# Optimization experiments

Measured on AMD Instinct MI355X. Metric: run time of the kernel, lower is better.

The kernel has to match this reference:

```python
import jax, jax.numpy as jnp
import numpy as np
import math

B, C, H, W = 8, 64, 256, 256
E, NH = 256, 8
HD = E // NH  # 32


def get_coords(h, w):
    xx, yy = jnp.meshgrid(jnp.arange(h, dtype=jnp.float32), jnp.arange(w, dtype=jnp.float32), indexing='ij')
    return jnp.stack((xx.reshape(-1), yy.reshape(-1)), axis=-1)  # [N, 2]


def setup_inputs() -> dict:
    key = jax.random.key(0)
    ks = jax.random.split(key, 12)
    def xavier(k, shape):
        fan_out, fan_in = shape
        a = math.sqrt(6.0 / (fan_in + fan_out))
        return jax.random.uniform(k, shape, jnp.float32, -a, a)
    x = jax.random.normal(ks[0], (B, C, H, W), jnp.float32)
    z = jax.random.normal(ks[1], (B, C), jnp.float32)
    pos = jax.random.uniform(ks[2], (B, NH, 2), jnp.float32) * (H - 1)
    Wq = xavier(ks[3], (E, C)); bq = jnp.zeros((E,), jnp.float32)
    Wk = xavier(ks[4], (E, C)); bk = jnp.zeros((E,), jnp.float32)
    Wv = xavier(ks[5], (E, C)); bv = jnp.zeros((E,), jnp.float32)
    Wp = xavier(ks[6], (HD, 2)); bp = jax.random.uniform(ks[7], (HD,), jnp.float32, -1.0, 1.0) / math.sqrt(2.0)
    return {"x": x, "z": z, "pos": pos, "Wq": Wq, "bq": bq, "Wk": Wk, "bk": bk,
            "Wv": Wv, "bv": bv, "Wp": Wp, "bp": bp}


def reference(x, z, pos, Wq, bq, Wk, bk, Wv, bv, Wp, bp):
    b, c, h, w = x.shape
    n = h * w
    x_flat = x.reshape(b, c, n).transpose(0, 2, 1)          # [B, N, C]
    pos_grid = get_coords(h, w)                              # [N, 2]
    q = (z @ Wq.T + bq).reshape(b, NH, HD)                   # [B, H, hd]
    k = (x_flat @ Wk.T + bk).reshape(b, n, NH, HD)           # [B, N, H, hd]
    # relative-position modulation of keys
    rel = pos_grid[None, :, None, :] - pos[:, None, :, :]    # [B, N, H, 2]
    qxk = rel @ Wp.T + bp                                    # [B, N, H, hd]
    k = k * qxk
    v = x_flat @ Wv.T + bv                                   # [B, N, E]
    attn_logits = jnp.einsum('bhc,bnhc->bnh', q, k) / math.sqrt(HD)
    attention = jax.nn.softmax(attn_logits, axis=1)          # softmax over N
    pos_out = jnp.einsum('bnh,nx->bhx', attention, pos_grid) # [B, H, 2]
    values = jnp.einsum('bnh,bnc->bhc', attention, v)        # [B, H, E]
    return (values, pos_out)
```

## Files before the change

### kernel.cpp

```cpp
#include <hip/hip_runtime.h>

#define NN    65536
#define NSUB  128
#define NBLK  (NN/NSUB)

typedef short bf16x8 __attribute__((ext_vector_type(8)));
typedef float f32x4v __attribute__((ext_vector_type(4)));
typedef unsigned short ushort_t;
typedef unsigned int uint_t;

#define XHI_B  0
#define XLO_B  18432
#define SLICE  4608
#define LGSTR  28
#define PSTR   40
#define PST_OFF 1536
#define RED_B  36864
#define SMEM_BYTES 37248

#define WTHI_B  0
#define WTLO_B  32768
#define CJ_B    65536
#define PM_B    66304
#define PL_B    197376
#define PSP_B   328448
#define PSX_B   590592
#define Q_B     8979200
#define QSTR    68

__device__ __forceinline__ uint_t bf16_rne_bits(float f) {
  uint_t u = __float_as_uint(f);
  return (u + 0x7FFFu + ((u >> 16) & 1u)) >> 16;
}
__device__ __forceinline__ uint_t cvt_pk_bf16(float a, float b) {
  uint_t r;
  asm("v_cvt_pk_bf16_f32 %0, %1, %2" : "=v"(r) : "v"(a), "v"(b));
  return r;
}
template <int CTRL, int RMASK = 0xf>
__device__ __forceinline__ float dpp_add(float x) {
  int t = __builtin_amdgcn_update_dpp(0, __float_as_int(x), CTRL, RMASK, 0xf, false);
  return x + __int_as_float(t);
}
template <int CTRL, int RMASK = 0xf>
__device__ __forceinline__ float dpp_maxs(float x) {
  int t = __builtin_amdgcn_update_dpp((int)0xFF800000u, __float_as_int(x), CTRL, RMASK, 0xf, false);
  return fmaxf(x, __int_as_float(t));
}
__device__ __forceinline__ float half_sum(float x) {
  x = dpp_add<0x111>(x); x = dpp_add<0x112>(x); x = dpp_add<0x114>(x);
  x = dpp_add<0x118>(x); x = dpp_add<0x142, 0xA>(x);
  return x;
}
__device__ __forceinline__ float half_max(float x) {
  x = dpp_maxs<0x111>(x); x = dpp_maxs<0x112>(x); x = dpp_maxs<0x114>(x);
  x = dpp_maxs<0x118>(x); x = dpp_maxs<0x142, 0xA>(x);
  return x;
}

__global__ __launch_bounds__(64) void prep_kernel(
    const float* __restrict__ z,  const float* __restrict__ Wq, const float* __restrict__ bq,
    const float* __restrict__ Wk, const float* __restrict__ bk,
    const float* __restrict__ Wp, const float* __restrict__ bp,
    ushort_t* __restrict__ WThi, ushort_t* __restrict__ WTlo, float* __restrict__ Cj)
{
  const int h = blockIdx.x, b = blockIdx.y, t = threadIdx.x;
  __shared__ float q[32];
  if (t < 32) {
    const int e = h*32 + t;
    float a = bq[e];
    const float* zr = z + b*64;
    const float* wr = Wq + e*64;
    #pragma unroll 8
    for (int c = 0; c < 64; ++c) a += zr[c]*wr[c];
    q[t] = a;
  }
  __syncthreads();
  const int c = t;
  float w[3] = {0.f, 0.f, 0.f};
  #pragma unroll 4
  for (int hd = 0; hd < 32; ++hd) {
    const float qk = q[hd] * Wk[(h*32+hd)*64 + c];
    w[0] += qk * bp[hd];
    w[1] += qk * Wp[hd*2+0];
    w[2] += qk * Wp[hd*2+1];
  }
  #pragma unroll
  for (int j = 0; j < 3; ++j) {
    const int coeff = h*3 + j;
    const uint_t hb = bf16_rne_bits(w[j]);
    const float  fh = __uint_as_float(hb << 16);
    const uint_t lb = bf16_rne_bits(w[j] - fh);
    WThi[(b*32 + coeff)*64 + c] = (ushort_t)hb;
    WTlo[(b*32 + coeff)*64 + c] = (ushort_t)lb;
  }
  if (h == 0) {
    #pragma unroll
    for (int r = 0; r < 8; ++r) {
      WThi[(b*32 + 24 + r)*64 + c] = 0;
      WTlo[(b*32 + 24 + r)*64 + c] = 0;
    }
  }
  if (t < 3) {
    float s = 0.f;
    for (int hd = 0; hd < 32; ++hd) {
      const float m = (t == 0) ? bp[hd] : Wp[hd*2 + (t-1)];
      s += q[hd] * m * bk[h*32+hd];
    }
    Cj[b*24 + h*3 + t] = s;
  }
}

__global__ __launch_bounds__(256, 4) void main_kernel(
    const float* __restrict__ x, const float* __restrict__ pos,
    const ushort_t* __restrict__ WThi, const ushort_t* __restrict__ WTlo,
    const float* __restrict__ Cj,
    float* __restrict__ Pm, float* __restrict__ Pl,
    float* __restrict__ Psp, float* __restrict__ Psx)
{
  extern __shared__ char smc[];
  float* red = (float*)(smc + RED_B);
  const int t   = threadIdx.x;
  const int blk = blockIdx.x;
  const int b   = blockIdx.y;
  const int n0  = blk * NSUB;
  const int w   = t >> 6, lid = t & 63;
  const int c0  = lid & 15, q4 = lid >> 4;
  char* slice = smc + XLO_B + w*SLICE;

  bf16x8 bh[2][2], bl[2][2];
  {
    const ushort_t* wtb_h = WThi + b*2048;
    const ushort_t* wtb_l = WTlo + b*2048;
    #pragma unroll
    for (int nt = 0; nt < 2; ++nt)
      #pragma unroll
      for (int ks = 0; ks < 2; ++ks) {
        const int off = (nt*16 + c0)*64 + ks*32 + q4*8;
        bh[nt][ks] = *(const bf16x8*)(wtb_h + off);
        bl[nt][ks] = *(const bf16x8*)(wtb_l + off);
      }
  }

  {
    const int qd  = lid & 7;
    const int g   = lid >> 3;
    const int swz = (4*w + (qd >> 1)) & 7;
    const int chnk = (g ^ swz) * 16;
    const float* xg = x + (size_t)b*64*NN + (size_t)g*8*NN + n0 + w*32 + 4*qd;
    f32x4v v[8];
    #pragma unroll
    for (int j = 0; j < 8; ++j) v[j] = *(const f32x4v*)(xg + (size_t)j*NN);
    #pragma unroll
    for (int i = 0; i < 4; ++i) {
      uint_t H[4], L[4];
      #pragma unroll
      for (int jp = 0; jp < 4; ++jp) {
        const float f0 = v[2*jp][i], f1 = v[2*jp+1][i];
        const uint_t hpk = cvt_pk_bf16(f0, f1);
        const float h0 = __uint_as_float(hpk << 16);
        const float h1 = __uint_as_float(hpk & 0xFFFF0000u);
        const uint_t l0 = __float_as_uint(f0 - h0);
        const uint_t l1 = __float_as_uint(f1 - h1);
        H[jp] = hpk;
        L[jp] = __builtin_amdgcn_perm(l1, l0, 0x07060302u);
      }
      const int row = w*32 + 4*qd + i;
      char* dh = smc + XHI_B + row*144 + chnk;
      char* dl = smc + XLO_B + row*144 + chnk;
      *(uint4*)dh = make_uint4(H[0], H[1], H[2], H[3]);
      *(uint4*)dl = make_uint4(L[0], L[1], L[2], L[3]);
    }
  }

  const int hg  = lid >> 5;
  const int pxl = lid & 31;
  float cj[12];
  {
    const float* cjp = Cj + b*24 + hg*12;
    #pragma unroll
    for (int k = 0; k < 12; ++k) cj[k] = cjp[k];
  }
  const int gx = blk >> 1;
  float rxh[4], py[4];
  #pragma unroll
  for (int hl = 0; hl < 4; ++hl) {
    const int h = hg*4 + hl;
    rxh[hl] = (float)gx - pos[(b*8+h)*2 + 0];
    py[hl]  = pos[(b*8+h)*2 + 1];
  }

  f32x4v acc[2][2];
  #pragma unroll
  for (int mt = 0; mt < 2; ++mt) { acc[mt][0] = (f32x4v)0.f; acc[mt][1] = (f32x4v)0.f; }
  {
    #pragma unroll
    for (int mt = 0; mt < 2; ++mt) {
      const int row  = w*32 + mt*16 + c0;
      const int srow = (4*w + 2*mt + (c0 >> 3)) & 7;
      const int ch0  = (q4 ^ srow) * 16;
      const char* rh = smc + XHI_B + row*144;
      const char* rl = smc + XLO_B + row*144;
      bf16x8 ah0 = *(const bf16x8*)(rh + ch0);
      bf16x8 ah1 = *(const bf16x8*)(rh + (ch0 ^ 64));
      bf16x8 al0 = *(const bf16x8*)(rl + ch0);
      bf16x8 al1 = *(const bf16x8*)(rl + (ch0 ^ 64));
      #pragma unroll
      for (int nt = 0; nt < 2; ++nt) {
        f32x4v a = acc[mt][nt];
        a = __builtin_amdgcn_mfma_f32_16x16x32_bf16(ah0, bh[nt][0], a, 0, 0, 0);
        a = __builtin_amdgcn_mfma_f32_16x16x32_bf16(ah1, bh[nt][1], a, 0, 0, 0);
        a = __builtin_amdgcn_mfma_f32_16x16x32_bf16(ah0, bl[nt][0], a, 0, 0, 0);
        a = __builtin_amdgcn_mfma_f32_16x16x32_bf16(ah1, bl[nt][1], a, 0, 0, 0);
        a = __builtin_amdgcn_mfma_f32_16x16x32_bf16(al0, bh[nt][0], a, 0, 0, 0);
        a = __builtin_amdgcn_mfma_f32_16x16x32_bf16(al1, bh[nt][1], a, 0, 0, 0);
        acc[mt][nt] = a;
      }
    }
  }

  {
    float* lga_w = (float*)slice;
    #pragma unroll
    for (int mt = 0; mt < 2; ++mt)
      #pragma unroll
      for (int r = 0; r < 4; ++r) {
        const int prow = mt*16 + q4*4 + r;
        lga_w[prow*LGSTR + c0] = acc[mt][0][r];
        if (c0 < 8) lga_w[prow*LGSTR + 16 + c0] = acc[mt][1][r];
      }
  }

  float a12[12];
  {
    const float4* ap = (const float4*)((float*)slice + pxl*LGSTR + hg*12);
    #pragma unroll
    for (int r = 0; r < 3; ++r) *(float4*)(a12 + 4*r) = ap[r];
  }
  const float tf = (float)(((blk & 1) << 7) + w*32 + pxl);
  float lg[4];
  #pragma unroll
  for (int hl = 0; hl < 4; ++hl) {
    const float a0 = a12[hl*3+0] + cj[hl*3+0];
    const float a1 = a12[hl*3+1] + cj[hl*3+1];
    const float a2 = a12[hl*3+2] + cj[hl*3+2];
    lg[hl] = (a0 + rxh[hl]*a1 + (tf - py[hl])*a2) * 0.17677669529663687f;
  }

  #pragma unroll
  for (int hl = 0; hl < 4; ++hl) {
    const float m = half_max(lg[hl]);
    if ((lid & 31) == 31) red[w*8 + hg*4 + hl] = m;
  }
  __syncthreads();

  float p[4];
  #pragma unroll
  for (int hl = 0; hl < 4; ++hl) {
    const int h = hg*4 + hl;
    const float M = fmaxf(fmaxf(red[0*8+h], red[1*8+h]), fmaxf(red[2*8+h], red[3*8+h]));
    p[hl] = __expf(lg[hl] - M);
  }

  #pragma unroll
  for (int hl = 0; hl < 4; ++hl) {
    const float sp  = half_sum(p[hl]);
    const float spj = half_sum(p[hl] * tf);
    if ((lid & 31) == 31) {
      red[32 + w*8 + hg*4 + hl] = sp;
      red[64 + w*8 + hg*4 + hl] = spj;
    }
  }
  {
    ushort_t* pls = (ushort_t*)slice;
    #pragma unroll
    for (int hl = 0; hl < 4; ++hl) {
      const int h = hg*4 + hl;
      const uint_t hb = bf16_rne_bits(p[hl]);
      const float  hf = __uint_as_float(hb << 16);
      const uint_t lb = __float_as_uint(p[hl] - hf) >> 16;
      pls[h*PSTR + pxl]     = (ushort_t)hb;
      pls[(h+8)*PSTR + pxl] = (ushort_t)lb;
    }
  }

  {
    const ushort_t* pls = (const ushort_t*)slice;
    const bf16x8 afr = *(const bf16x8*)(pls + c0*PSTR + q4*8);
    const int srow_b = (4*w + q4) & 7;
    float* pst = (float*)(slice + PST_OFF);
    #pragma unroll
    for (int nt = 0; nt < 4; ++nt) {
      const int gch  = nt*2 + (c0 >> 3);
      const char* base = smc + XHI_B + (w*32 + q4*8)*144 + ((gch ^ srow_b)*16) + (c0 & 7)*2;
      bf16x8 bfr;
      #pragma unroll
      for (int j = 0; j < 8; ++j) bfr[j] = *(const short*)(base + j*144);
      f32x4v accB = __builtin_amdgcn_mfma_f32_16x16x32_bf16(afr, bfr, (f32x4v)0.f, 0, 0, 0);
      #pragma unroll
      for (int r = 0; r < 4; ++r) {
        const float o = __shfl_xor(accB[r], 32, 64);
        if (q4 < 2) pst[(q4*4 + r)*64 + nt*16 + c0] = accB[r] + o;
      }
    }
  }
  __syncthreads();

  if (t < 8) {
    const int base = (b*NBLK + blk)*8 + t;
    const float M  = fmaxf(fmaxf(red[0*8+t], red[8+t]), fmaxf(red[16+t], red[24+t]));
    const float L  = red[32+t] + red[40+t] + red[48+t] + red[56+t];
    const float SJ = red[64+t] + red[72+t] + red[80+t] + red[88+t];
    Pm[base] = M;
    Pl[base] = L;
    Psp[base*2+0] = (float)gx * L;
    Psp[base*2+1] = SJ;
  }
  {
    const size_t pb64 = ((size_t)(b*NBLK + blk))*8*64;
    #pragma unroll
    for (int r = 0; r < 2; ++r) {
      const int idx = t + 256*r;
      float s = 0.f;
      #pragma unroll
      for (int w2 = 0; w2 < 4; ++w2)
        s += *(const float*)(smc + XLO_B + w2*SLICE + PST_OFF + idx*4);
      Psx[pb64 + idx] = s;
    }
  }
}

__global__ __launch_bounds__(256) void reduce1_kernel(
    const float* __restrict__ Pm, const float* __restrict__ Pl,
    const float* __restrict__ Psp, const float* __restrict__ Psx,
    float* __restrict__ Q)
{
  const int g = blockIdx.x, h = blockIdx.y, b = blockIdx.z, t = threadIdx.x;
  __shared__ float al[64];
  __shared__ float mgs;
  __shared__ float sums[3];
  __shared__ float sxl[256];
  const int base = (b*NBLK + g*64)*8 + h;

  float m_t = -1e30f;
  if (t < 64) {
    m_t = Pm[base + t*8];
    float mm = m_t;
    #pragma unroll
    for (int off = 32; off >= 1; off >>= 1) mm = fmaxf(mm, __shfl_xor(mm, off, 64));
    if (t == 0) mgs = mm;
  }
  __syncthreads();
  const float Mg = mgs;
  if (t < 64) {
    const float a = __expf(m_t - Mg);
    al[t] = a;
    float lt = Pl[base + t*8] * a;
    float sx = Psp[(base + t*8)*2 + 0] * a;
    float sy = Psp[(base + t*8)*2 + 1] * a;
    #pragma unroll
    for (int off = 32; off >= 1; off >>= 1) {
      lt += __shfl_xor(lt, off, 64);
      sx += __shfl_xor(sx, off, 64);
      sy += __shfl_xor(sy, off, 64);
    }
    if (t == 0) { sums[0] = lt; sums[1] = sx; sums[2] = sy; }
  }
  __syncthreads();
  {
    const int c = t & 63, g2 = t >> 6;
    float acc = 0.f;
    #pragma unroll
    for (int i = 0; i < 16; ++i) {
      const int k = g2*16 + i;
      acc += al[k] * Psx[(size_t)(base + k*8)*64 + c];
    }
    sxl[g2*64 + c] = acc;
  }
  __syncthreads();
  float* q = Q + ((b*8 + h)*8 + g)*QSTR;
  if (t < 64) q[4+t] = sxl[t] + sxl[64+t] + sxl[128+t] + sxl[192+t];
  if (t == 0) { q[0] = Mg; q[1] = sums[0]; q[2] = sums[1]; q[3] = sums[2]; }
}

__global__ __launch_bounds__(64) void reduce2_kernel(
    const float* __restrict__ Q, const float* __restrict__ Wv, const float* __restrict__ bv,
    float* __restrict__ out)
{
  const int h = blockIdx.x, b = blockIdx.y, t = threadIdx.x;
  __shared__ float qm[8], bl[8], l8[8], sx8[8], sy8[8];
  __shared__ float SXs[64];
  const float* qb = Q + ((b*8 + h)*8)*QSTR;

  if (t < 8) qm[t] = qb[t*QSTR + 0];
  __syncthreads();
  float M = qm[0];
  #pragma unroll
  for (int g = 1; g < 8; ++g) M = fmaxf(M, qm[g]);
  if (t < 8) {
    const float be = __expf(qm[t] - M);
    bl[t]  = be;
    l8[t]  = be * qb[t*QSTR + 1];
    sx8[t] = be * qb[t*QSTR + 2];
    sy8[t] = be * qb[t*QSTR + 3];
  }
  __syncthreads();
  float L = 0.f;
  #pragma unroll
  for (int g = 0; g < 8; ++g) L += l8[g];
  const float invL = 1.0f / L;
  {
    float s = 0.f;
    #pragma unroll
    for (int g = 0; g < 8; ++g) s += bl[g] * qb[g*QSTR + 4 + t];
    SXs[t] = s * invL;
  }
  __syncthreads();

  #pragma unroll
  for (int r = 0; r < 4; ++r) {
    const int e = t + 64*r;
    float v = bv[e];
    const float* wvr = Wv + e*64;
    #pragma unroll 8
    for (int c = 0; c < 64; ++c) v += wvr[c] * SXs[c];
    out[(b*8 + h)*256 + e] = v;
  }
  if (t == 0) {
    float spx = 0.f, spy = 0.f;
    #pragma unroll
    for (int g = 0; g < 8; ++g) { spx += sx8[g]; spy += sy8[g]; }
    out[16384 + (b*8 + h)*2 + 0] = spx * invL;
    out[16384 + (b*8 + h)*2 + 1] = spy * invL;
  }
}

extern "C" void kernel_launch(void* const* d_in, const int* in_sizes, int n_in,
                              void* d_out, int out_size, void* d_ws, size_t ws_size,
                              hipStream_t stream)
{
  const float* x   = (const float*)d_in[0];
  const float* z   = (const float*)d_in[1];
  const float* pos = (const float*)d_in[2];
  const float* Wq  = (const float*)d_in[3];
  const float* bq  = (const float*)d_in[4];
  const float* Wk  = (const float*)d_in[5];
  const float* bk  = (const float*)d_in[6];
  const float* Wv  = (const float*)d_in[7];
  const float* bv  = (const float*)d_in[8];
  const float* Wp  = (const float*)d_in[9];
  const float* bp  = (const float*)d_in[10];
  float* out = (float*)d_out;
  char*  wsb = (char*)d_ws;

  ushort_t* WThi = (ushort_t*)(wsb + WTHI_B);
  ushort_t* WTlo = (ushort_t*)(wsb + WTLO_B);
  float* Cj  = (float*)(wsb + CJ_B);
  float* Pm  = (float*)(wsb + PM_B);
  float* Pl  = (float*)(wsb + PL_B);
  float* Psp = (float*)(wsb + PSP_B);
  float* Psx = (float*)(wsb + PSX_B);
  float* Q   = (float*)(wsb + Q_B);

  prep_kernel   <<<dim3(8,8),    64,  0,          stream>>>(z, Wq, bq, Wk, bk, Wp, bp, WThi, WTlo, Cj);
  main_kernel   <<<dim3(NBLK,8), 256, SMEM_BYTES, stream>>>(x, pos, WThi, WTlo, Cj, Pm, Pl, Psp, Psx);
  reduce1_kernel<<<dim3(8,8,8),  256, 0,          stream>>>(Pm, Pl, Psp, Psx, Q);
  reduce2_kernel<<<dim3(8,8),    64,  0,          stream>>>(Q, Wv, bv, out);
}
```

Measured before the change: 236.8 us.

## Make main kernel persistent over eight tiles with double-buffered LDS and prefetch

Each block now handles eight consecutive 128-pixel tiles instead of one. It prefetches the next tile's x values into registers while computing the current one, and alternates between two LDS buffers. This amortizes the per-block setup (weight fragments, Cj, pos loads) and overlaps global loads with MFMA and softmax work. In exchange the grid shrinks to 512 blocks, LDS per block doubles, and occupancy drops to two blocks per CU.

```diff
diff --git a/kernel.cpp b/kernel.cpp
--- a/kernel.cpp
+++ b/kernel.cpp
@@ -3,20 +3,21 @@
 #define NN    65536
 #define NSUB  128
 #define NBLK  (NN/NSUB)
+#define NTILE 8
 
 typedef short bf16x8 __attribute__((ext_vector_type(8)));
 typedef float f32x4v __attribute__((ext_vector_type(4)));
 typedef unsigned short ushort_t;
 typedef unsigned int uint_t;
 
-#define XHI_B  0
-#define XLO_B  18432
-#define SLICE  4608
-#define LGSTR  28
-#define PSTR   40
+#define BUFSZ   36864
+#define XLO_OFF 18432
+#define SLICE   4608
+#define LGSTR   28
+#define PSTR    40
 #define PST_OFF 1536
-#define RED_B  36864
-#define SMEM_BYTES 37248
+#define RED_B   73728
+#define SMEM_BYTES 74112
 
 #define WTHI_B  0
 #define WTLO_B  32768
@@ -111,7 +112,7 @@
   }
 }
 
-__global__ __launch_bounds__(256, 4) void main_kernel(
+__global__ __launch_bounds__(256, 2) void main_kernel(
     const float* __restrict__ x, const float* __restrict__ pos,
     const ushort_t* __restrict__ WThi, const ushort_t* __restrict__ WTlo,
     const float* __restrict__ Cj,
@@ -120,13 +121,12 @@
 {
   extern __shared__ char smc[];
   float* red = (float*)(smc + RED_B);
-  const int t   = threadIdx.x;
-  const int blk = blockIdx.x;
-  const int b   = blockIdx.y;
-  const int n0  = blk * NSUB;
-  const int w   = t >> 6, lid = t & 63;
-  const int c0  = lid & 15, q4 = lid >> 4;
-  char* slice = smc + XLO_B + w*SLICE;
+  const int t    = threadIdx.x;
+  const int blk0 = blockIdx.x;
+  const int b    = blockIdx.y;
+  const int w    = t >> 6, lid = t & 63;
+  const int c0   = lid & 15, q4 = lid >> 4;
+  const int hg   = lid >> 5, pxl = lid & 31;
 
   bf16x8 bh[2][2], bl[2][2];
   {
@@ -142,15 +142,37 @@
       }
   }
 
+  float cj[12];
   {
-    const int qd  = lid & 7;
-    const int g   = lid >> 3;
-    const int swz = (4*w + (qd >> 1)) & 7;
-    const int chnk = (g ^ swz) * 16;
-    const float* xg = x + (size_t)b*64*NN + (size_t)g*8*NN + n0 + w*32 + 4*qd;
-    f32x4v v[8];
-    #pragma unroll
-    for (int j = 0; j < 8; ++j) v[j] = *(const f32x4v*)(xg + (size_t)j*NN);
+    const float* cjp = Cj + b*24 + hg*12;
+    #pragma unroll
+    for (int k = 0; k < 12; ++k) cj[k] = cjp[k];
+  }
+  float posx[4], py[4];
+  #pragma unroll
+  for (int hl = 0; hl < 4; ++hl) {
+    const int h = hg*4 + hl;
+    posx[hl] = pos[(b*8+h)*2 + 0];
+    py[hl]   = pos[(b*8+h)*2 + 1];
+  }
+
+  const int qd  = lid & 7;
+  const int g   = lid >> 3;
+  const int swz = (4*w + (qd >> 1)) & 7;
+  const int chnk = (g ^ swz) * 16;
+  const float* xg = x + (size_t)b*64*NN + (size_t)g*8*NN
+                      + (size_t)blk0*NTILE*NSUB + w*32 + 4*qd;
+  f32x4v v[8];
+  #pragma unroll
+  for (int j = 0; j < 8; ++j) v[j] = *(const f32x4v*)(xg + (size_t)j*NN);
+
+  for (int it = 0; it < NTILE; ++it) {
+    const int blk = blk0*NTILE + it;
+    char* bufb  = smc + (it & 1)*BUFSZ;
+    char* xhiB  = bufb;
+    char* xloB  = bufb + XLO_OFF;
+    char* slice = xloB + w*SLICE;
+
     #pragma unroll
     for (int i = 0; i < 4; ++i) {
       uint_t H[4], L[4];
@@ -166,41 +188,26 @@
         L[jp] = __builtin_amdgcn_perm(l1, l0, 0x07060302u);
       }
       const int row = w*32 + 4*qd + i;
-      char* dh = smc + XHI_B + row*144 + chnk;
-      char* dl = smc + XLO_B + row*144 + chnk;
-      *(uint4*)dh = make_uint4(H[0], H[1], H[2], H[3]);
-      *(uint4*)dl = make_uint4(L[0], L[1], L[2], L[3]);
-    }
-  }
-
-  const int hg  = lid >> 5;
-  const int pxl = lid & 31;
-  float cj[12];
-  {
-    const float* cjp = Cj + b*24 + hg*12;
-    #pragma unroll
-    for (int k = 0; k < 12; ++k) cj[k] = cjp[k];
-  }
-  const int gx = blk >> 1;
-  float rxh[4], py[4];
-  #pragma unroll
-  for (int hl = 0; hl < 4; ++hl) {
-    const int h = hg*4 + hl;
-    rxh[hl] = (float)gx - pos[(b*8+h)*2 + 0];
-    py[hl]  = pos[(b*8+h)*2 + 1];
-  }
-
-  f32x4v acc[2][2];
-  #pragma unroll
-  for (int mt = 0; mt < 2; ++mt) { acc[mt][0] = (f32x4v)0.f; acc[mt][1] = (f32x4v)0.f; }
-  {
+      *(uint4*)(xhiB + row*144 + chnk) = make_uint4(H[0], H[1], H[2], H[3]);
+      *(uint4*)(xloB + row*144 + chnk) = make_uint4(L[0], L[1], L[2], L[3]);
+    }
+
+    if (it + 1 < NTILE) {
+      xg += NSUB;
+      #pragma unroll
+      for (int j = 0; j < 8; ++j) v[j] = *(const f32x4v*)(xg + (size_t)j*NN);
+    }
+
+    f32x4v acc[2][2];
+    #pragma unroll
+    for (int mt = 0; mt < 2; ++mt) { acc[mt][0] = (f32x4v)0.f; acc[mt][1] = (f32x4v)0.f; }
     #pragma unroll
     for (int mt = 0; mt < 2; ++mt) {
       const int row  = w*32 + mt*16 + c0;
       const int srow = (4*w + 2*mt + (c0 >> 3)) & 7;
       const int ch0  = (q4 ^ srow) * 16;
-      const char* rh = smc + XHI_B + row*144;
-      const char* rl = smc + XLO_B + row*144;
+      const char* rh = xhiB + row*144;
+      const char* rl = xloB + row*144;
       bf16x8 ah0 = *(const bf16x8*)(rh + ch0);
       bf16x8 ah1 = *(const bf16x8*)(rh + (ch0 ^ 64));
       bf16x8 al0 = *(const bf16x8*)(rl + ch0);
@@ -217,115 +224,116 @@
         acc[mt][nt] = a;
       }
     }
-  }
-
-  {
-    float* lga_w = (float*)slice;
-    #pragma unroll
-    for (int mt = 0; mt < 2; ++mt)
-      #pragma unroll
-      for (int r = 0; r < 4; ++r) {
-        const int prow = mt*16 + q4*4 + r;
-        lga_w[prow*LGSTR + c0] = acc[mt][0][r];
-        if (c0 < 8) lga_w[prow*LGSTR + 16 + c0] = acc[mt][1][r];
-      }
-  }
-
-  float a12[12];
-  {
-    const float4* ap = (const float4*)((float*)slice + pxl*LGSTR + hg*12);
-    #pragma unroll
-    for (int r = 0; r < 3; ++r) *(float4*)(a12 + 4*r) = ap[r];
-  }
-  const float tf = (float)(((blk & 1) << 7) + w*32 + pxl);
-  float lg[4];
-  #pragma unroll
-  for (int hl = 0; hl < 4; ++hl) {
-    const float a0 = a12[hl*3+0] + cj[hl*3+0];
-    const float a1 = a12[hl*3+1] + cj[hl*3+1];
-    const float a2 = a12[hl*3+2] + cj[hl*3+2];
-    lg[hl] = (a0 + rxh[hl]*a1 + (tf - py[hl])*a2) * 0.17677669529663687f;
-  }
-
-  #pragma unroll
-  for (int hl = 0; hl < 4; ++hl) {
-    const float m = half_max(lg[hl]);
-    if ((lid & 31) == 31) red[w*8 + hg*4 + hl] = m;
-  }
-  __syncthreads();
-
-  float p[4];
-  #pragma unroll
-  for (int hl = 0; hl < 4; ++hl) {
-    const int h = hg*4 + hl;
-    const float M = fmaxf(fmaxf(red[0*8+h], red[1*8+h]), fmaxf(red[2*8+h], red[3*8+h]));
-    p[hl] = __expf(lg[hl] - M);
-  }
-
-  #pragma unroll
-  for (int hl = 0; hl < 4; ++hl) {
-    const float sp  = half_sum(p[hl]);
-    const float spj = half_sum(p[hl] * tf);
-    if ((lid & 31) == 31) {
-      red[32 + w*8 + hg*4 + hl] = sp;
-      red[64 + w*8 + hg*4 + hl] = spj;
-    }
-  }
-  {
-    ushort_t* pls = (ushort_t*)slice;
+
+    {
+      float* lga_w = (float*)slice;
+      #pragma unroll
+      for (int mt = 0; mt < 2; ++mt)
+        #pragma unroll
+        for (int r = 0; r < 4; ++r) {
+          const int prow = mt*16 + q4*4 + r;
+          lga_w[prow*LGSTR + c0] = acc[mt][0][r];
+          if (c0 < 8) lga_w[prow*LGSTR + 16 + c0] = acc[mt][1][r];
+        }
+    }
+
+    float a12[12];
+    {
+      const float4* ap = (const float4*)((float*)slice + pxl*LGSTR + hg*12);
+      #pragma unroll
+      for (int r = 0; r < 3; ++r) *(float4*)(a12 + 4*r) = ap[r];
+    }
+    const float gxf = (float)(blk >> 1);
+    const float tf  = (float)(((blk & 1) << 7) + w*32 + pxl);
+    float lg[4];
+    #pragma unroll
+    for (int hl = 0; hl < 4; ++hl) {
+      const float a0 = a12[hl*3+0] + cj[hl*3+0];
+      const float a1 = a12[hl*3+1] + cj[hl*3+1];
+      const float a2 = a12[hl*3+2] + cj[hl*3+2];
+      lg[hl] = (a0 + (gxf - posx[hl])*a1 + (tf - py[hl])*a2) * 0.17677669529663687f;
+    }
+
+    #pragma unroll
+    for (int hl = 0; hl < 4; ++hl) {
+      const float m = half_max(lg[hl]);
+      if ((lid & 31) == 31) red[w*8 + hg*4 + hl] = m;
+    }
+    __syncthreads();
+
+    float p[4];
     #pragma unroll
     for (int hl = 0; hl < 4; ++hl) {
       const int h = hg*4 + hl;
-      const uint_t hb = bf16_rne_bits(p[hl]);
-      const float  hf = __uint_as_float(hb << 16);
-      const uint_t lb = __float_as_uint(p[hl] - hf) >> 16;
-      pls[h*PSTR + pxl]     = (ushort_t)hb;
-      pls[(h+8)*PSTR + pxl] = (ushort_t)lb;
-    }
-  }
-
-  {
-    const ushort_t* pls = (const ushort_t*)slice;
-    const bf16x8 afr = *(const bf16x8*)(pls + c0*PSTR + q4*8);
-    const int srow_b = (4*w + q4) & 7;
-    float* pst = (float*)(slice + PST_OFF);
-    #pragma unroll
-    for (int nt = 0; nt < 4; ++nt) {
-      const int gch  = nt*2 + (c0 >> 3);
-      const char* base = smc + XHI_B + (w*32 + q4*8)*144 + ((gch ^ srow_b)*16) + (c0 & 7)*2;
-      bf16x8 bfr;
-      #pragma unroll
-      for (int j = 0; j < 8; ++j) bfr[j] = *(const short*)(base + j*144);
-      f32x4v accB = __builtin_amdgcn_mfma_f32_16x16x32_bf16(afr, bfr, (f32x4v)0.f, 0, 0, 0);
-      #pragma unroll
-      for (int r = 0; r < 4; ++r) {
-        const float o = __shfl_xor(accB[r], 32, 64);
-        if (q4 < 2) pst[(q4*4 + r)*64 + nt*16 + c0] = accB[r] + o;
-      }
-    }
-  }
-  __syncthreads();
-
-  if (t < 8) {
-    const int base = (b*NBLK + blk)*8 + t;
-    const float M  = fmaxf(fmaxf(red[0*8+t], red[8+t]), fmaxf(red[16+t], red[24+t]));
-    const float L  = red[32+t] + red[40+t] + red[48+t] + red[56+t];
-    const float SJ = red[64+t] + red[72+t] + red[80+t] + red[88+t];
-    Pm[base] = M;
-    Pl[base] = L;
-    Psp[base*2+0] = (float)gx * L;
-    Psp[base*2+1] = SJ;
-  }
-  {
-    const size_t pb64 = ((size_t)(b*NBLK + blk))*8*64;
-    #pragma unroll
-    for (int r = 0; r < 2; ++r) {
-      const int idx = t + 256*r;
-      float s = 0.f;
-      #pragma unroll
-      for (int w2 = 0; w2 < 4; ++w2)
-        s += *(const float*)(smc + XLO_B + w2*SLICE + PST_OFF + idx*4);
-      Psx[pb64 + idx] = s;
+      const float M = fmaxf(fmaxf(red[0*8+h], red[1*8+h]), fmaxf(red[2*8+h], red[3*8+h]));
+      p[hl] = __expf(lg[hl] - M);
+    }
+
+    #pragma unroll
+    for (int hl = 0; hl < 4; ++hl) {
+      const float sp  = half_sum(p[hl]);
+      const float spj = half_sum(p[hl] * tf);
+      if ((lid & 31) == 31) {
+        red[32 + w*8 + hg*4 + hl] = sp;
+        red[64 + w*8 + hg*4 + hl] = spj;
+      }
+    }
+    {
+      ushort_t* pls = (ushort_t*)slice;
+      #pragma unroll
+      for (int hl = 0; hl < 4; ++hl) {
+        const int h = hg*4 + hl;
+        const uint_t hb = bf16_rne_bits(p[hl]);
+        const float  hf = __uint_as_float(hb << 16);
+        const uint_t lb = __float_as_uint(p[hl] - hf) >> 16;
+        pls[h*PSTR + pxl]     = (ushort_t)hb;
+        pls[(h+8)*PSTR + pxl] = (ushort_t)lb;
+      }
+    }
+
+    {
+      const ushort_t* pls = (const ushort_t*)slice;
+      const bf16x8 afr = *(const bf16x8*)(pls + c0*PSTR + q4*8);
+      const int srow_b = (4*w + q4) & 7;
+      float* pst = (float*)(slice + PST_OFF);
+      #pragma unroll
+      for (int nt = 0; nt < 4; ++nt) {
+        const int gch  = nt*2 + (c0 >> 3);
+        const char* base = xhiB + (w*32 + q4*8)*144 + ((gch ^ srow_b)*16) + (c0 & 7)*2;
+        bf16x8 bfr;
+        #pragma unroll
+        for (int j = 0; j < 8; ++j) bfr[j] = *(const short*)(base + j*144);
+        f32x4v accB = __builtin_amdgcn_mfma_f32_16x16x32_bf16(afr, bfr, (f32x4v)0.f, 0, 0, 0);
+        #pragma unroll
+        for (int r = 0; r < 4; ++r) {
+          const float o = __shfl_xor(accB[r], 32, 64);
+          if (q4 < 2) pst[(q4*4 + r)*64 + nt*16 + c0] = accB[r] + o;
+        }
+      }
+    }
+    __syncthreads();
+
+    if (t < 8) {
+      const int base = (b*NBLK + blk)*8 + t;
+      const float M  = fmaxf(fmaxf(red[0*8+t], red[8+t]), fmaxf(red[16+t], red[24+t]));
+      const float L  = red[32+t] + red[40+t] + red[48+t] + red[56+t];
+      const float SJ = red[64+t] + red[72+t] + red[80+t] + red[88+t];
+      Pm[base] = M;
+      Pl[base] = L;
+      Psp[base*2+0] = gxf * L;
+      Psp[base*2+1] = SJ;
+    }
+    {
+      const size_t pb64 = ((size_t)(b*NBLK + blk))*8*64;
+      #pragma unroll
+      for (int r = 0; r < 2; ++r) {
+        const int idx = t + 256*r;
+        float s = 0.f;
+        #pragma unroll
+        for (int w2 = 0; w2 < 4; ++w2)
+          s += *(const float*)(xloB + w2*SLICE + PST_OFF + idx*4);
+        Psx[pb64 + idx] = s;
+      }
     }
   }
 }
@@ -462,8 +470,11 @@
   float* Psx = (float*)(wsb + PSX_B);
   float* Q   = (float*)(wsb + Q_B);
 
-  prep_kernel   <<<dim3(8,8),    64,  0,          stream>>>(z, Wq, bq, Wk, bk, Wp, bp, WThi, WTlo, Cj);
-  main_kernel   <<<dim3(NBLK,8), 256, SMEM_BYTES, stream>>>(x, pos, WThi, WTlo, Cj, Pm, Pl, Psp, Psx);
-  reduce1_kernel<<<dim3(8,8,8),  256, 0,          stream>>>(Pm, Pl, Psp, Psx, Q);
-  reduce2_kernel<<<dim3(8,8),    64,  0,          stream>>>(Q, Wv, bv, out);
-}
+  (void)hipFuncSetAttribute((const void*)main_kernel,
+                            hipFuncAttributeMaxDynamicSharedMemorySize, SMEM_BYTES);
+
+  prep_kernel   <<<dim3(8,8),          64,  0,          stream>>>(z, Wq, bq, Wk, bk, Wp, bp, WThi, WTlo, Cj);
+  main_kernel   <<<dim3(NBLK/NTILE,8), 256, SMEM_BYTES, stream>>>(x, pos, WThi, WTlo, Cj, Pm, Pl, Psp, Psx);
+  reduce1_kernel<<<dim3(8,8,8),        256, 0,          stream>>>(Pm, Pl, Psp, Psx, Q);
+  reduce2_kernel<<<dim3(8,8),          64,  0,          stream>>>(Q, Wv, bv, out);
+}
```

Result: slower. 246.2 us (+4.0%).
